# Performance work log

Hardware: AMD Instinct MI355X
Metric: run time of the kernel (lower is better)

The kernel has to match this reference:

```python
import jax, jax.numpy as jnp
import numpy as np

OUTPUT_DIM = 1024  # init kwarg output_dim


def _adaptive_avg_pool_last(x, out_dim):
    """Faithful F.adaptive_avg_pool1d over the last axis (static shapes)."""
    in_dim = x.shape[-1]
    if in_dim % out_dim == 0:
        k = in_dim // out_dim
        return x.reshape(x.shape[:-1] + (out_dim, k)).mean(axis=-1)
    # generic case: window i covers [floor(i*In/Out), ceil((i+1)*In/Out))
    idx = np.arange(out_dim)
    starts = (idx * in_dim) // out_dim
    ends = -((-(idx + 1) * in_dim) // out_dim)
    W = np.zeros((in_dim, out_dim), dtype=np.float32)
    for i in range(out_dim):
        W[starts[i]:ends[i], i] = 1.0 / (ends[i] - starts[i])
    return x @ jnp.asarray(W)


def _per_layer_gram(feat, output_dim):
    N, C, ph, pw = feat.shape
    P = ph * pw
    c_red = min(C, 64)
    f = feat.reshape(N, C, P).transpose(0, 2, 1)        # [N, P, C]
    f = _adaptive_avg_pool_last(f, c_red)               # [N, P, Cr] channel reduction
    fr = f.transpose(0, 2, 1)                           # [N, Cr, P]
    gram = jnp.einsum('ncp,ndp->ncd', fr, fr) / P       # [N, Cr, Cr] per-patch Gram
    return _adaptive_avg_pool_last(gram.reshape(N, c_red * c_red), output_dim)  # [N, output_dim]


def setup_inputs() -> dict:
    key = jax.random.key(0)
    k0, k1 = jax.random.split(key)
    feat0 = jax.random.normal(k0, (6272, 512, 3, 3), dtype=jnp.float32)
    feat1 = jax.random.normal(k1, (6272, 1024, 3, 3), dtype=jnp.float32)
    return {"feat0": feat0, "feat1": feat1}


def reference(feat0, feat1):
    # stack over layers -> [N, L=2, output_dim]
    return jnp.stack(
        [_per_layer_gram(feat0, OUTPUT_DIM), _per_layer_gram(feat1, OUTPUT_DIM)],
        axis=1,
    )
```

## Files before the change

### kernel.cpp

```cpp
#include <hip/hip_runtime.h>


#define N_SAMPLES 6272

typedef const __attribute__((address_space(1))) void* gas_ptr;
typedef __attribute__((address_space(3))) void* las_ptr;

__device__ __forceinline__ void load16_to_lds(const void* g, void* l) {
    __builtin_amdgcn_global_load_lds((gas_ptr)g, (las_ptr)l, 16, 0, 0);
}

template <int CH>
__global__ __launch_bounds__(256) void patchgram_layer(
    const float* __restrict__ src, float* __restrict__ out)
{
    constexpr int NF   = CH * 9;
    constexpr int NV4  = NF / 4;
    constexpr int GSH  = (CH == 1024) ? 2 : 1;
    constexpr int NRED = 64 << GSH;
    constexpr int K    = CH / 64;
    constexpr float SCALE = 1.0f / (36.0f * (float)(K * K));

    __shared__ float4 tile[NV4];
    __shared__ float4 fr4[64 * 3];
    __shared__ float4 B4[16 * 3];

    const int n = blockIdx.x;
    const int t = threadIdx.x;

    const float4* __restrict__ g = (const float4*)(src + (size_t)n * NF);
    for (int i = t; i < NV4; i += 256)
        load16_to_lds(&g[i], &tile[i]);
    __syncthreads();

    if (t < NRED) {
        const float4* __restrict__ tp = &tile[t * 9];
        float acc[9];
#pragma unroll
        for (int p = 0; p < 9; ++p) acc[p] = 0.f;
#pragma unroll
        for (int j = 0; j < 9; ++j) {
            const float4 v = tp[j];
            acc[(4 * j + 0) % 9] += v.x;
            acc[(4 * j + 1) % 9] += v.y;
            acc[(4 * j + 2) % 9] += v.z;
            acc[(4 * j + 3) % 9] += v.w;
        }
#pragma unroll
        for (int p = 0; p < 9; ++p) acc[p] += __shfl_xor(acc[p], 1);
        if (GSH == 2) {
#pragma unroll
            for (int p = 0; p < 9; ++p) acc[p] += __shfl_xor(acc[p], 2);
        }
        if ((t & ((1 << GSH) - 1)) == 0) {
            const int row = t >> GSH;
            fr4[row * 3 + 0] = make_float4(acc[0], acc[1], acc[2], acc[3]);
            fr4[row * 3 + 1] = make_float4(acc[4], acc[5], acc[6], acc[7]);
            fr4[row * 3 + 2] = make_float4(acc[8], 0.f, 0.f, 0.f);
        }
    }
    __syncthreads();

    if (t < 144) {
        const int dg = t / 9;
        const int p  = t - dg * 9;
        const float* fr = (const float*)fr4;
        ((float*)B4)[dg * 12 + p] =
            fr[(4 * dg + 0) * 12 + p] + fr[(4 * dg + 1) * 12 + p] +
            fr[(4 * dg + 2) * 12 + p] + fr[(4 * dg + 3) * 12 + p];
    }
    __syncthreads();

    const int c   = t >> 2;
    const int dgq = t & 3;
    const float4 a0 = fr4[c * 3 + 0];
    const float4 a1 = fr4[c * 3 + 1];
    const float4 a2 = fr4[c * 3 + 2];

    float4 o4;
    float* op = (float*)&o4;
#pragma unroll
    for (int j = 0; j < 4; ++j) {
        const int d = dgq * 4 + j;
        const float4 b0 = B4[d * 3 + 0];
        const float4 b1 = B4[d * 3 + 1];
        const float4 b2 = B4[d * 3 + 2];
        float s = a0.x * b0.x + a0.y * b0.y + a0.z * b0.z + a0.w * b0.w
                + a1.x * b1.x + a1.y * b1.y + a1.z * b1.z + a1.w * b1.w
                + a2.x * b2.x;
        op[j] = s * SCALE;
    }
    float4* o = (float4*)(out + (size_t)n * 2048 + c * 16 + dgq * 4);
    *o = o4;
}

extern "C" void kernel_launch(void* const* d_in, const int* in_sizes, int n_in,
                              void* d_out, int out_size, void* d_ws, size_t ws_size,
                              hipStream_t stream) {
    const float* f0 = (const float*)d_in[0];
    const float* f1 = (const float*)d_in[1];
    float* out = (float*)d_out;
    patchgram_layer<512><<<N_SAMPLES, 256, 0, stream>>>(f0, out);
    patchgram_layer<1024><<<N_SAMPLES, 256, 0, stream>>>(f1, out + 1024);
}
```

Before: 388.5 us.

## Load features directly into registers instead of staging through LDS

```diff
diff --git a/kernel.cpp b/kernel.cpp
--- a/kernel.cpp
+++ b/kernel.cpp
@@ -3,67 +3,53 @@
 
 #define N_SAMPLES 6272
 
-typedef const __attribute__((address_space(1))) void* gas_ptr;
-typedef __attribute__((address_space(3))) void* las_ptr;
-
-__device__ __forceinline__ void load16_to_lds(const void* g, void* l) {
-    __builtin_amdgcn_global_load_lds((gas_ptr)g, (las_ptr)l, 16, 0, 0);
-}
-
 template <int CH>
-__global__ __launch_bounds__(256) void patchgram_layer(
+__global__ __launch_bounds__(CH / 4) void patchgram_reg(
     const float* __restrict__ src, float* __restrict__ out)
 {
-    constexpr int NF   = CH * 9;
-    constexpr int NV4  = NF / 4;
-    constexpr int GSH  = (CH == 1024) ? 2 : 1;
-    constexpr int NRED = 64 << GSH;
-    constexpr int K    = CH / 64;
+    constexpr int T   = CH / 4;
+    constexpr int K   = CH / 64;
+    constexpr int TPR = K / 4;
     constexpr float SCALE = 1.0f / (36.0f * (float)(K * K));
 
-    __shared__ float4 tile[NV4];
     __shared__ float4 fr4[64 * 3];
     __shared__ float4 B4[16 * 3];
 
     const int n = blockIdx.x;
     const int t = threadIdx.x;
 
-    const float4* __restrict__ g = (const float4*)(src + (size_t)n * NF);
-    for (int i = t; i < NV4; i += 256)
-        load16_to_lds(&g[i], &tile[i]);
-    __syncthreads();
+    const float4* __restrict__ g =
+        (const float4*)(src + (size_t)n * (CH * 9)) + t * 9;
 
-    if (t < NRED) {
-        const float4* __restrict__ tp = &tile[t * 9];
-        float acc[9];
+    float acc[9];
 #pragma unroll
-        for (int p = 0; p < 9; ++p) acc[p] = 0.f;
+    for (int p = 0; p < 9; ++p) acc[p] = 0.f;
 #pragma unroll
-        for (int j = 0; j < 9; ++j) {
-            const float4 v = tp[j];
-            acc[(4 * j + 0) % 9] += v.x;
-            acc[(4 * j + 1) % 9] += v.y;
-            acc[(4 * j + 2) % 9] += v.z;
-            acc[(4 * j + 3) % 9] += v.w;
-        }
+    for (int j = 0; j < 9; ++j) {
+        const float4 v = g[j];
+        acc[(4 * j + 0) % 9] += v.x;
+        acc[(4 * j + 1) % 9] += v.y;
+        acc[(4 * j + 2) % 9] += v.z;
+        acc[(4 * j + 3) % 9] += v.w;
+    }
+
 #pragma unroll
-        for (int p = 0; p < 9; ++p) acc[p] += __shfl_xor(acc[p], 1);
-        if (GSH == 2) {
+    for (int p = 0; p < 9; ++p) acc[p] += __shfl_xor(acc[p], 1);
+    if (TPR == 4) {
 #pragma unroll
-            for (int p = 0; p < 9; ++p) acc[p] += __shfl_xor(acc[p], 2);
-        }
-        if ((t & ((1 << GSH) - 1)) == 0) {
-            const int row = t >> GSH;
-            fr4[row * 3 + 0] = make_float4(acc[0], acc[1], acc[2], acc[3]);
-            fr4[row * 3 + 1] = make_float4(acc[4], acc[5], acc[6], acc[7]);
-            fr4[row * 3 + 2] = make_float4(acc[8], 0.f, 0.f, 0.f);
-        }
+        for (int p = 0; p < 9; ++p) acc[p] += __shfl_xor(acc[p], 2);
+    }
+    if ((t & (TPR - 1)) == 0) {
+        const int row = t / TPR;
+        fr4[row * 3 + 0] = make_float4(acc[0], acc[1], acc[2], acc[3]);
+        fr4[row * 3 + 1] = make_float4(acc[4], acc[5], acc[6], acc[7]);
+        fr4[row * 3 + 2] = make_float4(acc[8], 0.f, 0.f, 0.f);
     }
     __syncthreads();
 
-    if (t < 144) {
-        const int dg = t / 9;
-        const int p  = t - dg * 9;
+    for (int i = t; i < 144; i += T) {
+        const int dg = i / 9;
+        const int p  = i - dg * 9;
         const float* fr = (const float*)fr4;
         ((float*)B4)[dg * 12 + p] =
             fr[(4 * dg + 0) * 12 + p] + fr[(4 * dg + 1) * 12 + p] +
@@ -71,27 +57,33 @@
     }
     __syncthreads();
 
-    const int c   = t >> 2;
-    const int dgq = t & 3;
+    constexpr int OPT = 1024 / T;
+    constexpr int GPR = 16 / OPT;
+    const int c     = t / GPR;
+    const int dbase = (t % GPR) * OPT;
+
     const float4 a0 = fr4[c * 3 + 0];
     const float4 a1 = fr4[c * 3 + 1];
     const float4 a2 = fr4[c * 3 + 2];
 
-    float4 o4;
-    float* op = (float*)&o4;
+    float o[OPT];
 #pragma unroll
-    for (int j = 0; j < 4; ++j) {
-        const int d = dgq * 4 + j;
+    for (int j = 0; j < OPT; ++j) {
+        const int d = dbase + j;
         const float4 b0 = B4[d * 3 + 0];
         const float4 b1 = B4[d * 3 + 1];
         const float4 b2 = B4[d * 3 + 2];
-        float s = a0.x * b0.x + a0.y * b0.y + a0.z * b0.z + a0.w * b0.w
-                + a1.x * b1.x + a1.y * b1.y + a1.z * b1.z + a1.w * b1.w
-                + a2.x * b2.x;
-        op[j] = s * SCALE;
+        o[j] = (a0.x * b0.x + a0.y * b0.y + a0.z * b0.z + a0.w * b0.w
+              + a1.x * b1.x + a1.y * b1.y + a1.z * b1.z + a1.w * b1.w
+              + a2.x * b2.x) * SCALE;
     }
-    float4* o = (float4*)(out + (size_t)n * 2048 + c * 16 + dgq * 4);
-    *o = o4;
+
+    float* obase = out + (size_t)n * 2048 + c * 16 + dbase;
+#pragma unroll
+    for (int q = 0; q < OPT / 4; ++q) {
+        ((float4*)obase)[q] =
+            make_float4(o[4 * q + 0], o[4 * q + 1], o[4 * q + 2], o[4 * q + 3]);
+    }
 }
 
 extern "C" void kernel_launch(void* const* d_in, const int* in_sizes, int n_in,
@@ -100,6 +92,6 @@
     const float* f0 = (const float*)d_in[0];
     const float* f1 = (const float*)d_in[1];
     float* out = (float*)d_out;
-    patchgram_layer<512><<<N_SAMPLES, 256, 0, stream>>>(f0, out);
-    patchgram_layer<1024><<<N_SAMPLES, 256, 0, stream>>>(f1, out + 1024);
+    patchgram_reg<512><<<N_SAMPLES, 128, 0, stream>>>(f0, out);
+    patchgram_reg<1024><<<N_SAMPLES, 256, 0, stream>>>(f1, out + 1024);
 }
```

Measured after the change: 386.3 us. Within noise of the previous version (-0.6%).
